# Kernel tuning notes

Measured on AMD Instinct MI355X. Metric: run time of the kernel, lower is better.

## Reference

```python
import jax, jax.numpy as jnp
import numpy as np

INPUT_DIM = 64
HIDDEN_DIM = 128
N_ROWS = 2_000_000
N_GROUPS = 2


def setup_inputs() -> dict:
    key = jax.random.key(0)
    k_x, k_T, k_w1, k_b1, k_w2, k_b2 = jax.random.split(key, 6)
    x = jax.random.normal(k_x, (N_ROWS, INPUT_DIM), dtype=jnp.float32)
    T = jax.random.randint(k_T, (N_ROWS,), 0, N_GROUPS, dtype=jnp.int64)
    # Linear params (torch convention: W @ x layout -> y = x @ W.T + b)
    lim1 = 1.0 / np.sqrt(INPUT_DIM)
    W1 = jax.random.uniform(k_w1, (HIDDEN_DIM, INPUT_DIM), jnp.float32, -lim1, lim1)
    b1 = jax.random.uniform(k_b1, (HIDDEN_DIM,), jnp.float32, -lim1, lim1)
    lim2 = 1.0 / np.sqrt(HIDDEN_DIM)
    W2 = jax.random.uniform(k_w2, (1, HIDDEN_DIM), jnp.float32, -lim2, lim2)
    b2 = jax.random.uniform(k_b2, (1,), jnp.float32, -lim2, lim2)
    return {"x": x, "T": T, "W1": W1, "b1": b1, "W2": W2, "b2": b2}


def reference(x, T, W1, b1, W2, b2):
    # s = f2(tanh(f1(x))).flatten()  -> [N]
    h = jnp.tanh(x @ W1.T + b1)                      # [N, H]
    s = (h @ W2.T + b2).reshape(-1)                  # [N]
    e = jnp.exp(s)                                   # faithful to torch.exp (unshifted)
    # group sums via segment_sum (2 groups), then gather-normalize per row
    sums = jax.ops.segment_sum(e, T, num_segments=N_GROUPS)  # [2]
    return e / sums[T]
```

## Files before the change

kernel.cpp:

```cpp
#include <hip/hip_runtime.h>
#include <math.h>

#define NROWS 2000000
#define IN_DIM 64
#define HID 128
#define NTILES (NROWS / 16)
#define BLOCK 256
#define NBLK 768
#define WPB (BLOCK / 64)

typedef _Float16 half8 __attribute__((ext_vector_type(8)));
typedef float f32x4 __attribute__((ext_vector_type(4)));

__device__ __forceinline__ float tanh_fast(float a) {
    float p = __expf(2.0f * a);
    float r = __builtin_amdgcn_rcpf(p + 1.0f);
    return fmaf(-2.0f, r, 1.0f);
}

__device__ __forceinline__ float dpp_row_sum16(float v) {
    int x;
    x = __float_as_int(v);
    v += __int_as_float(__builtin_amdgcn_update_dpp(0, x, 0x111, 0xf, 0xf, true));
    x = __float_as_int(v);
    v += __int_as_float(__builtin_amdgcn_update_dpp(0, x, 0x112, 0xf, 0xf, true));
    x = __float_as_int(v);
    v += __int_as_float(__builtin_amdgcn_update_dpp(0, x, 0x114, 0xf, 0xf, true));
    x = __float_as_int(v);
    v += __int_as_float(__builtin_amdgcn_update_dpp(0, x, 0x118, 0xf, 0xf, true));
    return v;
}

__device__ __forceinline__ void dma_tile(const float* __restrict__ xsrc,
                                         char* dst, int lane) {
    #pragma unroll
    for (int k = 0; k < 4; k++) {
        const int slot = k * 64 + lane;
        const int r = slot >> 4, cs = slot & 15;
        const int srcc = (r << 4) | (cs ^ (r & 7));
        __builtin_amdgcn_global_load_lds(
            (const __attribute__((address_space(1))) void*)(xsrc + srcc * 4),
            (__attribute__((address_space(3))) void*)(dst + k * 1024),
            16, 0, 0);
    }
}

__global__ void zero_sums_kernel(float* g) {
    if (threadIdx.x < 2) g[threadIdx.x] = 0.0f;
}

__global__ __launch_bounds__(BLOCK, 3) void fused_mfma_kernel(
    const float* __restrict__ x, const int* __restrict__ T,
    const float* __restrict__ W1, const float* __restrict__ b1,
    const float* __restrict__ W2, const float* __restrict__ b2,
    float* __restrict__ e_out, float* __restrict__ gsums)
{
    __shared__ char xbuf[WPB][2][4096];

    const int lane = threadIdx.x & 63;
    const int wv   = threadIdx.x >> 6;
    const int c16  = lane & 15;
    const int g4   = lane >> 4;

    half8 wreg[8][2];
    #pragma unroll
    for (int t = 0; t < 8; t++) {
        const int n = t * 16 + c16;
        #pragma unroll
        for (int c = 0; c < 2; c++) {
            const float* wp = W1 + n * IN_DIM + c * 32 + g4 * 8;
            half8 h;
            #pragma unroll
            for (int j = 0; j < 8; j++) h[j] = (_Float16)wp[j];
            wreg[t][c] = h;
        }
    }
    float b1v[8], w2v[8];
    #pragma unroll
    for (int t = 0; t < 8; t++) {
        b1v[t] = b1[t * 16 + c16];
        w2v[t] = W2[t * 16 + c16];
    }
    const float b2v = b2[0];

    char* bufA = &xbuf[wv][0][0];
    char* bufB = &xbuf[wv][1][0];

    const int gwave = blockIdx.x * WPB + wv;
    const int nwave = NBLK * WPB;

    float ls0 = 0.f, ls1 = 0.f;

    int tile = gwave;
    if (tile < NTILES) dma_tile(x + (size_t)tile * 1024, bufA, lane);

    const int c7 = c16 & 7;
    const int col0 = (2 * g4) ^ c7;
    const int col1 = (2 * g4 + 1) ^ c7;
    const int rb = c16 * 256;
    const int o0 = rb + col0 * 16;
    const int o1 = rb + col1 * 16;
    const int o2 = rb + (col0 + 8) * 16;
    const int o3 = rb + (col1 + 8) * 16;

    for (; tile < NTILES; tile += nwave) {
        asm volatile("s_waitcnt vmcnt(0)" ::: "memory");

        f32x4 a0 = *(const f32x4*)(bufA + o0);
        f32x4 a1 = *(const f32x4*)(bufA + o1);
        f32x4 a2 = *(const f32x4*)(bufA + o2);
        f32x4 a3 = *(const f32x4*)(bufA + o3);

        const int nt = tile + nwave;
        if (nt < NTILES) dma_tile(x + (size_t)nt * 1024, bufB, lane);

        half8 xf0, xf1;
        #pragma unroll
        for (int j = 0; j < 4; j++) {
            xf0[j]     = (_Float16)a0[j];
            xf0[4 + j] = (_Float16)a1[j];
            xf1[j]     = (_Float16)a2[j];
            xf1[4 + j] = (_Float16)a3[j];
        }

        f32x4 acc[8];
        #pragma unroll
        for (int t = 0; t < 8; t++) acc[t] = (f32x4){0.f, 0.f, 0.f, 0.f};
        #pragma unroll
        for (int t = 0; t < 8; t++) {
            acc[t] = __builtin_amdgcn_mfma_f32_16x16x32_f16(xf0, wreg[t][0], acc[t], 0, 0, 0);
            acc[t] = __builtin_amdgcn_mfma_f32_16x16x32_f16(xf1, wreg[t][1], acc[t], 0, 0, 0);
        }

        float sp0 = 0.f, sp1 = 0.f, sp2 = 0.f, sp3 = 0.f;
        #pragma unroll
        for (int t = 0; t < 8; t++) {
            sp0 = fmaf(tanh_fast(acc[t][0] + b1v[t]), w2v[t], sp0);
            sp1 = fmaf(tanh_fast(acc[t][1] + b1v[t]), w2v[t], sp1);
            sp2 = fmaf(tanh_fast(acc[t][2] + b1v[t]), w2v[t], sp2);
            sp3 = fmaf(tanh_fast(acc[t][3] + b1v[t]), w2v[t], sp3);
        }
        sp0 = dpp_row_sum16(sp0);
        sp1 = dpp_row_sum16(sp1);
        sp2 = dpp_row_sum16(sp2);
        sp3 = dpp_row_sum16(sp3);

        if (c16 == 15) {
            const int row0 = tile * 16 + g4 * 4;
            float e0 = __expf(sp0 + b2v);
            float e1 = __expf(sp1 + b2v);
            float e2 = __expf(sp2 + b2v);
            float e3 = __expf(sp3 + b2v);
            *(f32x4*)&e_out[row0] = (f32x4){e0, e1, e2, e3};
            int4 t4 = *(const int4*)&T[row0];
            if (t4.x == 0) ls0 += e0; else ls1 += e0;
            if (t4.y == 0) ls0 += e1; else ls1 += e1;
            if (t4.z == 0) ls0 += e2; else ls1 += e2;
            if (t4.w == 0) ls0 += e3; else ls1 += e3;
        }

        char* tmp = bufA; bufA = bufB; bufB = tmp;
    }

    #pragma unroll
    for (int off = 32; off > 0; off >>= 1) {
        ls0 += __shfl_down(ls0, off, 64);
        ls1 += __shfl_down(ls1, off, 64);
    }
    if (lane == 0) {
        atomicAdd(&gsums[0], ls0);
        atomicAdd(&gsums[1], ls1);
    }
}

__global__ __launch_bounds__(256) void normalize_kernel(
    float* __restrict__ e_out, const int* __restrict__ T,
    const float* __restrict__ gsums)
{
    const float inv0 = 1.0f / gsums[0];
    const float inv1 = 1.0f / gsums[1];
    const int n4 = NROWS / 4;
    const int stride = gridDim.x * blockDim.x;
    for (int i = blockIdx.x * blockDim.x + threadIdx.x; i < n4; i += stride) {
        float4 e = reinterpret_cast<const float4*>(e_out)[i];
        int4  t = reinterpret_cast<const int4*>(T)[i];
        e.x *= (t.x == 0) ? inv0 : inv1;
        e.y *= (t.y == 0) ? inv0 : inv1;
        e.z *= (t.z == 0) ? inv0 : inv1;
        e.w *= (t.w == 0) ? inv0 : inv1;
        reinterpret_cast<float4*>(e_out)[i] = e;
    }
}

extern "C" void kernel_launch(void* const* d_in, const int* in_sizes, int n_in,
                              void* d_out, int out_size, void* d_ws, size_t ws_size,
                              hipStream_t stream) {
    const float* x  = (const float*)d_in[0];
    const int*   T  = (const int*)d_in[1];
    const float* W1 = (const float*)d_in[2];
    const float* b1 = (const float*)d_in[3];
    const float* W2 = (const float*)d_in[4];
    const float* b2 = (const float*)d_in[5];
    float* e_out = (float*)d_out;
    float* gsums = (float*)d_ws;

    zero_sums_kernel<<<1, 64, 0, stream>>>(gsums);

    fused_mfma_kernel<<<NBLK, BLOCK, 0, stream>>>(x, T, W1, b1, W2, b2, e_out, gsums);

    normalize_kernel<<<2048, 256, 0, stream>>>(e_out, T, gsums);
}
```

Measured before the change: 179.1 us.

## Triple-buffer x tile DMA and fold tanh into exp2-based sigmoid algebra

Moves from double to triple buffering of the x tiles in LDS, issuing the prefetch two tiles ahead. It uses partial vmcnt waits so one tile's load stays in flight while the current tile is computed. It also rewrites tanh as 1-2/(1+e^{2a}) with the constants folded in: the bias is prescaled by 2*log2e, the output bias absorbs sum(w2), and exp2 is used directly. This is meant to hide global-load latency and cut ALU work, but it raises LDS use (fewer resident blocks possible) and relies on hand-counted vmcnt values, which can break if the compiler adds other loads such as the T load.

```diff
diff --git a/kernel.cpp b/kernel.cpp
--- a/kernel.cpp
+++ b/kernel.cpp
@@ -12,11 +12,14 @@
 typedef _Float16 half8 __attribute__((ext_vector_type(8)));
 typedef float f32x4 __attribute__((ext_vector_type(4)));
 
-__device__ __forceinline__ float tanh_fast(float a) {
-    float p = __expf(2.0f * a);
-    float r = __builtin_amdgcn_rcpf(p + 1.0f);
-    return fmaf(-2.0f, r, 1.0f);
-}
+#define TWO_LOG2E 2.885390081777927f
+#define LOG2E     1.4426950408889634f
+
+#if __has_builtin(__builtin_amdgcn_exp2f)
+#define EXP2F(x) __builtin_amdgcn_exp2f(x)
+#else
+#define EXP2F(x) __expf((x) * 0.6931471805599453f)
+#endif
 
 __device__ __forceinline__ float dpp_row_sum16(float v) {
     int x;
@@ -55,7 +58,7 @@
     const float* __restrict__ W2, const float* __restrict__ b2,
     float* __restrict__ e_out, float* __restrict__ gsums)
 {
-    __shared__ char xbuf[WPB][2][4096];
+    __shared__ char xbuf[WPB][3][4096];
 
     const int lane = threadIdx.x & 63;
     const int wv   = threadIdx.x >> 6;
@@ -75,16 +78,19 @@
             wreg[t][c] = h;
         }
     }
-    float b1v[8], w2v[8];
+    float d1v[8], w2v[8];
+    float w2loc = 0.f;
     #pragma unroll
     for (int t = 0; t < 8; t++) {
-        b1v[t] = b1[t * 16 + c16];
+        d1v[t] = TWO_LOG2E * b1[t * 16 + c16];
         w2v[t] = W2[t * 16 + c16];
-    }
-    const float b2v = b2[0];
-
-    char* bufA = &xbuf[wv][0][0];
-    char* bufB = &xbuf[wv][1][0];
+        w2loc += w2v[t];
+    }
+    const float Sconst = dpp_row_sum16(w2loc) + b2[0];
+
+    char* b0 = &xbuf[wv][0][0];
+    char* b1_ = &xbuf[wv][1][0];
+    char* b2_ = &xbuf[wv][2][0];
 
     const int gwave = blockIdx.x * WPB + wv;
     const int nwave = NBLK * WPB;
@@ -92,7 +98,13 @@
     float ls0 = 0.f, ls1 = 0.f;
 
     int tile = gwave;
-    if (tile < NTILES) dma_tile(x + (size_t)tile * 1024, bufA, lane);
+    dma_tile(x + (size_t)tile * 1024, b0, lane);
+    if (tile + nwave < NTILES) {
+        dma_tile(x + (size_t)(tile + nwave) * 1024, b1_, lane);
+        asm volatile("s_waitcnt vmcnt(4)" ::: "memory");
+    } else {
+        asm volatile("s_waitcnt vmcnt(0)" ::: "memory");
+    }
 
     const int c7 = c16 & 7;
     const int col0 = (2 * g4) ^ c7;
@@ -104,15 +116,10 @@
     const int o3 = rb + (col1 + 8) * 16;
 
     for (; tile < NTILES; tile += nwave) {
-        asm volatile("s_waitcnt vmcnt(0)" ::: "memory");
-
-        f32x4 a0 = *(const f32x4*)(bufA + o0);
-        f32x4 a1 = *(const f32x4*)(bufA + o1);
-        f32x4 a2 = *(const f32x4*)(bufA + o2);
-        f32x4 a3 = *(const f32x4*)(bufA + o3);
-
-        const int nt = tile + nwave;
-        if (nt < NTILES) dma_tile(x + (size_t)nt * 1024, bufB, lane);
+        f32x4 a0 = *(const f32x4*)(b0 + o0);
+        f32x4 a1 = *(const f32x4*)(b0 + o1);
+        f32x4 a2 = *(const f32x4*)(b0 + o2);
+        f32x4 a3 = *(const f32x4*)(b0 + o3);
 
         half8 xf0, xf1;
         #pragma unroll
@@ -135,10 +142,14 @@
         float sp0 = 0.f, sp1 = 0.f, sp2 = 0.f, sp3 = 0.f;
         #pragma unroll
         for (int t = 0; t < 8; t++) {
-            sp0 = fmaf(tanh_fast(acc[t][0] + b1v[t]), w2v[t], sp0);
-            sp1 = fmaf(tanh_fast(acc[t][1] + b1v[t]), w2v[t], sp1);
-            sp2 = fmaf(tanh_fast(acc[t][2] + b1v[t]), w2v[t], sp2);
-            sp3 = fmaf(tanh_fast(acc[t][3] + b1v[t]), w2v[t], sp3);
+            float r0 = __builtin_amdgcn_rcpf(EXP2F(fmaf(acc[t][0], TWO_LOG2E, d1v[t])) + 1.0f);
+            float r1 = __builtin_amdgcn_rcpf(EXP2F(fmaf(acc[t][1], TWO_LOG2E, d1v[t])) + 1.0f);
+            float r2 = __builtin_amdgcn_rcpf(EXP2F(fmaf(acc[t][2], TWO_LOG2E, d1v[t])) + 1.0f);
+            float r3 = __builtin_amdgcn_rcpf(EXP2F(fmaf(acc[t][3], TWO_LOG2E, d1v[t])) + 1.0f);
+            sp0 = fmaf(w2v[t], r0, sp0);
+            sp1 = fmaf(w2v[t], r1, sp1);
+            sp2 = fmaf(w2v[t], r2, sp2);
+            sp3 = fmaf(w2v[t], r3, sp3);
         }
         sp0 = dpp_row_sum16(sp0);
         sp1 = dpp_row_sum16(sp1);
@@ -147,19 +158,27 @@
 
         if (c16 == 15) {
             const int row0 = tile * 16 + g4 * 4;
-            float e0 = __expf(sp0 + b2v);
-            float e1 = __expf(sp1 + b2v);
-            float e2 = __expf(sp2 + b2v);
-            float e3 = __expf(sp3 + b2v);
+            int4 t4 = *(const int4*)&T[row0];
+            float e0 = EXP2F(fmaf(-2.0f * sp0, LOG2E, Sconst * LOG2E));
+            float e1 = EXP2F(fmaf(-2.0f * sp1, LOG2E, Sconst * LOG2E));
+            float e2 = EXP2F(fmaf(-2.0f * sp2, LOG2E, Sconst * LOG2E));
+            float e3 = EXP2F(fmaf(-2.0f * sp3, LOG2E, Sconst * LOG2E));
             *(f32x4*)&e_out[row0] = (f32x4){e0, e1, e2, e3};
-            int4 t4 = *(const int4*)&T[row0];
             if (t4.x == 0) ls0 += e0; else ls1 += e0;
             if (t4.y == 0) ls0 += e1; else ls1 += e1;
             if (t4.z == 0) ls0 += e2; else ls1 += e2;
             if (t4.w == 0) ls0 += e3; else ls1 += e3;
         }
 
-        char* tmp = bufA; bufA = bufB; bufB = tmp;
+        const int nt2 = tile + 2 * nwave;
+        if (nt2 < NTILES) {
+            dma_tile(x + (size_t)nt2 * 1024, b2_, lane);
+            asm volatile("s_waitcnt vmcnt(5)" ::: "memory");
+        } else {
+            asm volatile("s_waitcnt vmcnt(1)" ::: "memory");
+        }
+
+        char* tmp = b0; b0 = b1_; b1_ = b2_; b2_ = tmp;
     }
 
     #pragma unroll
```

Result: no change. 176.9 us (-1.3%).
